# Optimization experiments

Measured on AMD Instinct MI355X. Metric: run time of the kernel, lower is better.

Reference implementation:

```python
import math
import jax, jax.numpy as jnp
import numpy as np

N = 1600; C_IN = 16; HID = 64; OUT = 64; D_K = 8; N_HEADS = 8
CUTS = 8; NUM_RBF = 8; RBF_PROJ = 4; RADIUS = 6.0; ALPHA = 3.0

def leaky(x):
    return jnp.where(x >= 0, x, 0.2 * x)

def group_norm(x, gamma, beta, groups=4, eps=1e-5):
    # x: [N, C]; torch GroupNorm applied on [1, C, N]: stats over (C/groups, N) per group
    n, c = x.shape
    xg = x.T.reshape(groups, -1)
    mu = jnp.mean(xg, axis=1, keepdims=True)
    var = jnp.mean((xg - mu) ** 2, axis=1, keepdims=True)
    xn = ((xg - mu) * jax.lax.rsqrt(var + eps)).reshape(c, n).T
    return xn * gamma + beta

def setup_inputs():
    key = jax.random.key(0)
    ks = jax.random.split(key, 32)
    def rn(k, shape, s=0.1):
        return (jax.random.normal(k, shape) * s).astype(jnp.float32)
    return {
        "points": jax.random.normal(ks[0], (N, 3), jnp.float32),
        "nuv": jax.random.normal(ks[1], (N, 3, 3), jnp.float32),
        "features": jax.random.normal(ks[2], (N, C_IN), jnp.float32),
        "w_in1": rn(ks[3], (HID, C_IN)), "b_in1": rn(ks[4], (HID,)),
        "w_in2": rn(ks[5], (HID, HID)), "b_in2": rn(ks[6], (HID,)),
        "g_in": 1.0 + rn(ks[7], (HID,)), "be_in": rn(ks[8], (HID,)),
        "wq": rn(ks[9], (HID, HID)), "bq": rn(ks[10], (HID,)),
        "wk": rn(ks[11], (HID, HID)), "bk": rn(ks[12], (HID,)),
        "wv": rn(ks[13], (HID, HID)), "bv": rn(ks[14], (HID,)),
        "conv_w1": rn(ks[15], (CUTS, 4 + RBF_PROJ), 0.5),
        "conv_b1": jnp.abs(rn(ks[16], (CUTS,), 0.5)),
        "conv_w2": rn(ks[17], (HID, CUTS), 0.3), "conv_b2": rn(ks[18], (HID,), 0.3),
        "rbf_log_sigma": jnp.log(jnp.asarray(0.6 * 2.0 / (NUM_RBF - 1), jnp.float32)),
        "rbf_a": rn(ks[19], (RBF_PROJ, NUM_RBF), 0.3), "rbf_b": rn(ks[20], (RBF_PROJ,), 0.1),
        "rbf_centers": jnp.linspace(0.0, 2.0, NUM_RBF, dtype=jnp.float32),
        "w_o1": rn(ks[21], (OUT, HID)), "b_o1": rn(ks[22], (OUT,)),
        "w_o2": rn(ks[23], (OUT, OUT)), "b_o2": rn(ks[24], (OUT,)),
        "g_out": 1.0 + rn(ks[25], (OUT,)), "be_out": rn(ks[26], (OUT,)),
        "w_res": rn(ks[27], (OUT, C_IN)), "b_res": rn(ks[28], (OUT,)),
    }

def reference(points, nuv, features, w_in1, b_in1, w_in2, b_in2, g_in, be_in,
              wq, bq, wk, bk, wv, bv, conv_w1, conv_b1, conv_w2, conv_b2,
              rbf_log_sigma, rbf_a, rbf_b, rbf_centers,
              w_o1, b_o1, w_o2, b_o2, g_out, be_out, w_res, b_res):
    # point-wise MLP + GroupNorm
    h = leaky(features @ w_in1.T + b_in1)
    h = leaky(h @ w_in2.T + b_in2)
    h = group_norm(h, g_in, be_in)
    Q = h @ wq.T + bq
    K = h @ wk.T + bk
    V = h @ wv.T + bv
    pts = points / (math.sqrt(2.0) * RADIUS)
    diff = pts[None, :, :] - pts[:, None, :]            # [N, N, 3] = x_j - x_i
    n_i = nuv[:, 0, :]
    n_j = jax.lax.stop_gradient(n_i)                    # j-side normals are detached in the original
    ndot = jnp.einsum("ia,ja->ij", n_i, n_j)            # <n_i, n_j>
    d2 = jnp.sum(diff ** 2, axis=-1) * (2.0 - ndot) ** 2  # pseudo-geodesic squared distance
    W = (1.0 + d2 / ALPHA) ** (-ALPHA)                  # geodesic window weight
    d2_safe = jnp.where(d2 > 0, d2, 1.0)
    base_d = jnp.where(d2 > 0, jnp.sqrt(d2_safe), 0.0)  # safe sqrt (finite grad at 0)
    sigma = jnp.maximum(jnp.exp(rbf_log_sigma), 1e-6)
    R = jnp.exp(-((base_d[:, :, None] - rbf_centers) ** 2) / (2.0 * sigma ** 2))  # [N,N,NUM_RBF]
    R_proj = R @ rbf_a.T + rbf_b                        # [N, N, RBF_PROJ]
    X_loc = jnp.einsum("iab,ijb->ija", nuv, diff)       # local tangent-frame coords [N,N,3]
    X = jnp.concatenate([X_loc, ndot[:, :, None], R_proj], axis=-1)  # [N, N, 4+RBF_PROJ]
    F1 = jax.nn.relu(X @ conv_w1.T + conv_b1)           # shared conv layer-1 [N, N, CUTS]
    scale = 1.0 / math.sqrt(D_K)
    heads = []
    for h_id in range(N_HEADS):
        s = slice(h_id * D_K, (h_id + 1) * D_K)
        Fh = jax.nn.relu(F1 @ conv_w2[s].T + conv_b2[s])      # per-head conv weights [N, N, D_K]
        S = (Q[:, s] @ K[:, s].T) * scale                     # attention logits [N, N]
        P = jax.nn.softmax(S, axis=1) * W                     # softmax over j, fused with window
        heads.append(jnp.einsum("ij,ijc,jc->ic", P, Fh, V[:, s]))
    agg = jnp.concatenate(heads, axis=1)                      # [N, HID]
    o = leaky(agg @ w_o1.T + b_o1)
    o = leaky(o @ w_o2.T + b_o2)
    o = group_norm(o, g_out, be_out)
    return o + features @ w_res.T + b_res
```

## Files before the change

kernel.cpp:

```cpp
#include <hip/hip_runtime.h>

#define NPTS 1600
#define NCHUNK 10
#define CHUNKJ 160
#define TILE 32
#define QS (0.35355339059327373f*1.4426950408889634f)
#define PSCALE 0.11785113019775793f

__device__ __forceinline__ float leaky(float x){ return x >= 0.f ? x : 0.2f*x; }
__device__ __forceinline__ float d4(float4 a, float4 b){ return a.x*b.x + a.y*b.y + a.z*b.z + a.w*b.w; }

__global__ __launch_bounds__(256) void k_in(
    const float* __restrict__ feat, const float* __restrict__ w1, const float* __restrict__ b1,
    const float* __restrict__ w2, const float* __restrict__ b2,
    const float* __restrict__ conv_w1, const float* __restrict__ conv_b1,
    const float* __restrict__ rbf_a, const float* __restrict__ rbf_b,
    float* __restrict__ h2out, float* __restrict__ stats,
    float* __restrict__ wrg, float* __restrict__ b1pg)
{
  __shared__ float sh[4][64];
  __shared__ float sred[4][8];
  int t = threadIdx.x, w = t>>6, c = t&63;
  int i = blockIdx.x*4 + w;

  if (blockIdx.x == 0) {
    if (t < 64) {
      int cc = t>>3, k = t&7; float s = 0.f;
      #pragma unroll
      for (int p=0;p<4;p++) s += conv_w1[cc*8+4+p]*rbf_a[p*8+k];
      wrg[t] = s;
    } else if (t < 72) {
      int cc = t-64; float s = conv_b1[cc];
      #pragma unroll
      for (int p=0;p<4;p++) s += conv_w1[cc*8+4+p]*rbf_b[p];
      b1pg[cc] = s;
    }
  }

  const float4* f4 = (const float4*)(feat + i*16);
  float4 f0=f4[0], f1v=f4[1], f2v=f4[2], f3v=f4[3];
  const float4* w1r = (const float4*)(w1 + c*16);
  float h1 = b1[c] + d4(f0,w1r[0]) + d4(f1v,w1r[1]) + d4(f2v,w1r[2]) + d4(f3v,w1r[3]);
  h1 = leaky(h1);
  sh[w][c] = h1;
  __syncthreads();
  float hh = b2[c];
  #pragma unroll
  for (int k4=0;k4<16;k4++){
    float4 hv = *(const float4*)&sh[w][k4*4];
    hh += d4(hv, *(const float4*)&w2[c*64 + k4*4]);
  }
  hh = leaky(hh);
  h2out[i*64+c] = hh;

  float s = hh, qq = hh*hh;
  s += __shfl_xor(s,1);  qq += __shfl_xor(qq,1);
  s += __shfl_xor(s,2);  qq += __shfl_xor(qq,2);
  s += __shfl_xor(s,4);  qq += __shfl_xor(qq,4);
  s += __shfl_xor(s,8);  qq += __shfl_xor(qq,8);
  if ((c&15)==0){ int g=c>>4; sred[w][g]=s; sred[w][4+g]=qq; }
  __syncthreads();
  if (t<8){ float v2 = sred[0][t]+sred[1][t]+sred[2][t]+sred[3][t]; atomicAdd(&stats[t], v2); }
}

__global__ __launch_bounds__(256) void k_qkv(
  const float* __restrict__ h2, const float* __restrict__ stats,
  const float* __restrict__ g_in, const float* __restrict__ be_in,
  const float* __restrict__ wq, const float* __restrict__ bq,
  const float* __restrict__ wk, const float* __restrict__ bk,
  const float* __restrict__ wv, const float* __restrict__ bv,
  float* __restrict__ Q, float* __restrict__ K, float* __restrict__ V)
{
  __shared__ float sh[4][64];
  int t=threadIdx.x, w=t>>6, c=t&63;
  int i = blockIdx.x*4 + w;
  int g = c>>4;
  const float inv = 1.f/25600.f;
  float mu = stats[g]*inv;
  float var = stats[4+g]*inv - mu*mu;
  float rs = rsqrtf(var + 1e-5f);
  float hn = (h2[i*64+c]-mu)*rs*g_in[c] + be_in[c];
  sh[w][c] = hn;
  __syncthreads();
  float q=bq[c], k=bk[c], v=bv[c];
  #pragma unroll
  for (int k4=0;k4<16;k4++){
    float4 hv = *(const float4*)&sh[w][k4*4];
    q += d4(hv, *(const float4*)&wq[c*64+k4*4]);
    k += d4(hv, *(const float4*)&wk[c*64+k4*4]);
    v += d4(hv, *(const float4*)&wv[c*64+k4*4]);
  }
  Q[i*64+c] = q*QS;
  K[i*64+c] = k;
  V[i*64+c] = v;
}

__global__ __launch_bounds__(256) void k_pair(
  const float* __restrict__ Qm, const float* __restrict__ Km, const float* __restrict__ Vm,
  const float* __restrict__ pts, const float* __restrict__ nuv,
  const float* __restrict__ w1, const float* __restrict__ wrg, const float* __restrict__ b1pg,
  const float* __restrict__ w2g, const float* __restrict__ b2g,
  const float* __restrict__ rbf_ls, const float* __restrict__ ceng,
  float* __restrict__ part)
{
  __shared__ __align__(16) float sQ[16][68];
  __shared__ __align__(16) float sWX[16][36];
  __shared__ __align__(16) float sKx[TILE][68];
  __shared__ __align__(16) float sVx[TILE][68];
  __shared__ __align__(16) float sPt[TILE][4];
  __shared__ __align__(16) float sNj[TILE][4];
  __shared__ __align__(16) float sRed[4][16][72];

  int t = threadIdx.x;
  int r = t & 15, jl = t >> 4;
  int bx = blockIdx.x;
  int rb = bx % 100, jc = bx / 100;
  int I0 = rb*16, J0 = jc*CHUNKJ;
  int i = I0 + r;

  {
    int row = t >> 4, col = (t & 15) << 2;
    *(float4*)&sQ[row][col] = *(const float4*)&Qm[(I0+row)*64 + col];
  }
  if (t < 128) {
    int r2 = t >> 3, cc = t & 7;
    int ib = (I0+r2)*9;
    #pragma unroll
    for (int b=0;b<3;b++)
      sWX[r2][cc*4+b] = w1[cc*8+0]*nuv[ib+b] + w1[cc*8+1]*nuv[ib+3+b] + w1[cc*8+2]*nuv[ib+6+b];
    sWX[r2][cc*4+3] = w1[cc*8+3];
  }

  float ls = rbf_ls[0];
  float sig = fmaxf(expf(ls), 1e-6f);
  float mexp = -1.4426950408889634f/(2.f*sig*sig);
  float cen[8];
  #pragma unroll
  for (int k=0;k<8;k++) cen[k] = ceng[k];

  float pix = pts[i*3+0]*PSCALE, piy = pts[i*3+1]*PSCALE, piz = pts[i*3+2]*PSCALE;
  float nix = nuv[i*9+0], niy = nuv[i*9+1], niz = nuv[i*9+2];

  float acc[64];
  #pragma unroll
  for (int o=0;o<64;o++) acc[o] = 0.f;
  float lh[8];
  #pragma unroll
  for (int h=0;h<8;h++) lh[h] = 0.f;

  #pragma unroll 1
  for (int tb=0; tb<CHUNKJ; tb+=TILE) {
    int jbase = J0 + tb;
    __syncthreads();
    #pragma unroll
    for (int qq2=0; qq2<2; qq2++) {
      int idx4 = t + qq2*256;
      int row = idx4 >> 4, col = (idx4 & 15) << 2;
      *(float4*)&sKx[row][col] = *(const float4*)&Km[(jbase+row)*64+col];
      *(float4*)&sVx[row][col] = *(const float4*)&Vm[(jbase+row)*64+col];
    }
    if (t < TILE) {
      int j = jbase + t;
      sPt[t][0]=pts[j*3+0]*PSCALE; sPt[t][1]=pts[j*3+1]*PSCALE; sPt[t][2]=pts[j*3+2]*PSCALE;
      sNj[t][0]=nuv[j*9+0]; sNj[t][1]=nuv[j*9+1]; sNj[t][2]=nuv[j*9+2];
    }
    __syncthreads();

    float F1[2][8], Wv[2];
    #pragma unroll
    for (int jj=0;jj<2;jj++) {
      int jloc = jl + (jj<<4);
      float dx = sPt[jloc][0]-pix, dy = sPt[jloc][1]-piy, dz = sPt[jloc][2]-piz;
      float ndot = nix*sNj[jloc][0] + niy*sNj[jloc][1] + niz*sNj[jloc][2];
      float d2r = dx*dx + dy*dy + dz*dz;
      float wf = 2.f - ndot;
      float d2 = d2r*wf*wf;
      float tp = fmaf(d2, 0.3333333333333333f, 1.f);
      Wv[jj] = __builtin_amdgcn_rcpf(tp*tp*tp);
      float dd = __builtin_amdgcn_sqrtf(d2);
      float R[8];
      #pragma unroll
      for (int k=0;k<8;k++){ float u = dd - cen[k]; R[k] = __builtin_amdgcn_exp2f(u*u*mexp); }
      #pragma unroll
      for (int cc=0;cc<8;cc++) {
        float4 wx = *(const float4*)&sWX[r][cc*4];
        float p = b1pg[cc] + wx.x*dx + wx.y*dy + wx.z*dz + wx.w*ndot;
        #pragma unroll
        for (int k=0;k<8;k++) p = fmaf(R[k], wrg[cc*8+k], p);
        F1[jj][cc] = fmaxf(p, 0.f);
      }
    }

    #pragma unroll
    for (int h=0;h<8;h++) {
      float4 q0 = *(const float4*)&sQ[r][h*8];
      float4 q1 = *(const float4*)&sQ[r][h*8+4];
      float ew[2];
      float va[2][8];
      #pragma unroll
      for (int jj=0;jj<2;jj++) {
        int jloc = jl + (jj<<4);
        float4 k0 = *(const float4*)&sKx[jloc][h*8];
        float4 k1 = *(const float4*)&sKx[jloc][h*8+4];
        float S = d4(q0,k0) + d4(q1,k1);
        float e = __builtin_amdgcn_exp2f(S);
        lh[h] += e;
        ew[jj] = e * Wv[jj];
        float4 v0 = *(const float4*)&sVx[jloc][h*8];
        float4 v1 = *(const float4*)&sVx[jloc][h*8+4];
        va[jj][0]=v0.x; va[jj][1]=v0.y; va[jj][2]=v0.z; va[jj][3]=v0.w;
        va[jj][4]=v1.x; va[jj][5]=v1.y; va[jj][6]=v1.z; va[jj][7]=v1.w;
      }
      #pragma unroll
      for (int cc=0;cc<8;cc++) {
        float b2v = b2g[h*8+cc];
        float w2v[8];
        #pragma unroll
        for (int b=0;b<8;b++) w2v[b] = w2g[(h*8+cc)*8+b];
        #pragma unroll
        for (int jj=0;jj<2;jj++) {
          float fh = b2v;
          #pragma unroll
          for (int b=0;b<8;b++) fh = fmaf(F1[jj][b], w2v[b], fh);
          fh = fmaxf(fh, 0.f);
          acc[h*8+cc] = fmaf(ew[jj]*fh, va[jj][cc], acc[h*8+cc]);
        }
      }
    }
  }

  #pragma unroll
  for (int o=0;o<64;o++){ acc[o] += __shfl_xor(acc[o],16); acc[o] += __shfl_xor(acc[o],32); }
  #pragma unroll
  for (int h=0;h<8;h++){ lh[h] += __shfl_xor(lh[h],16); lh[h] += __shfl_xor(lh[h],32); }
  __syncthreads();
  int wv = t >> 6, lane = t & 63;
  if (lane < 16) {
    #pragma unroll
    for (int o=0;o<64;o++) sRed[wv][lane][o] = acc[o];
    #pragma unroll
    for (int h=0;h<8;h++) sRed[wv][lane][64+h] = lh[h];
  }
  __syncthreads();
  for (int v2 = t; v2 < 16*72; v2 += 256) {
    int rr = v2/72, o = v2 - rr*72;
    float s = sRed[0][rr][o]+sRed[1][rr][o]+sRed[2][rr][o]+sRed[3][rr][o];
    part[(jc*NPTS + I0 + rr)*72 + o] = s;
  }
}

__global__ __launch_bounds__(256) void k_agg(
  const float* __restrict__ part, const float* __restrict__ w_o1, const float* __restrict__ b_o1,
  const float* __restrict__ w_o2, const float* __restrict__ b_o2,
  float* __restrict__ o2b, float* __restrict__ stats)
{
  __shared__ float sh[4][64];
  __shared__ float sred[4][8];
  int t = threadIdx.x, w = t>>6, c = t&63;
  int i = blockIdx.x*4 + w;
  int h = c>>3;
  float a = 0.f, L = 0.f;
  #pragma unroll 1
  for (int jc=0;jc<NCHUNK;jc++){
    const float* p = part + (jc*NPTS + i)*72;
    a += p[c]; L += p[64+h];
  }
  float agg = a / L;
  sh[w][c] = agg; __syncthreads();
  float o1 = b_o1[c];
  #pragma unroll
  for (int k4=0;k4<16;k4++){
    float4 hv = *(const float4*)&sh[w][k4*4];
    o1 += d4(hv, *(const float4*)&w_o1[c*64+k4*4]);
  }
  o1 = leaky(o1);
  __syncthreads();
  sh[w][c] = o1; __syncthreads();
  float o2 = b_o2[c];
  #pragma unroll
  for (int k4=0;k4<16;k4++){
    float4 hv = *(const float4*)&sh[w][k4*4];
    o2 += d4(hv, *(const float4*)&w_o2[c*64+k4*4]);
  }
  o2 = leaky(o2);
  o2b[i*64+c] = o2;

  float s = o2, qq = o2*o2;
  s += __shfl_xor(s,1);  qq += __shfl_xor(qq,1);
  s += __shfl_xor(s,2);  qq += __shfl_xor(qq,2);
  s += __shfl_xor(s,4);  qq += __shfl_xor(qq,4);
  s += __shfl_xor(s,8);  qq += __shfl_xor(qq,8);
  if ((c&15)==0){ int g=c>>4; sred[w][g]=s; sred[w][4+g]=qq; }
  __syncthreads();
  if (t<8){ float v2 = sred[0][t]+sred[1][t]+sred[2][t]+sred[3][t]; atomicAdd(&stats[8+t], v2); }
}

__global__ __launch_bounds__(256) void k_out(
  const float* __restrict__ o2b, const float* __restrict__ stats,
  const float* __restrict__ g_out, const float* __restrict__ be_out,
  const float* __restrict__ feat, const float* __restrict__ w_res, const float* __restrict__ b_res,
  float* __restrict__ out)
{
  int t = threadIdx.x, w = t>>6, c = t&63;
  int i = blockIdx.x*4 + w;
  int g = c>>4;
  const float inv = 1.f/25600.f;
  float mu = stats[8+g]*inv;
  float var = stats[12+g]*inv - mu*mu;
  float rs = rsqrtf(var + 1e-5f);
  float on = (o2b[i*64+c]-mu)*rs*g_out[c] + be_out[c];
  const float4* f4 = (const float4*)(feat + i*16);
  const float4* wr = (const float4*)(w_res + c*16);
  float res = b_res[c] + d4(f4[0],wr[0]) + d4(f4[1],wr[1]) + d4(f4[2],wr[2]) + d4(f4[3],wr[3]);
  out[i*64+c] = on + res;
}

extern "C" void kernel_launch(void* const* d_in, const int* in_sizes, int n_in,
                              void* d_out, int out_size, void* d_ws, size_t ws_size,
                              hipStream_t stream) {
  const float* points  = (const float*)d_in[0];
  const float* nuv     = (const float*)d_in[1];
  const float* feat    = (const float*)d_in[2];
  const float* w_in1   = (const float*)d_in[3];
  const float* b_in1   = (const float*)d_in[4];
  const float* w_in2   = (const float*)d_in[5];
  const float* b_in2   = (const float*)d_in[6];
  const float* g_in    = (const float*)d_in[7];
  const float* be_in   = (const float*)d_in[8];
  const float* wq      = (const float*)d_in[9];
  const float* bq      = (const float*)d_in[10];
  const float* wk      = (const float*)d_in[11];
  const float* bk      = (const float*)d_in[12];
  const float* wv      = (const float*)d_in[13];
  const float* bv      = (const float*)d_in[14];
  const float* conv_w1 = (const float*)d_in[15];
  const float* conv_b1 = (const float*)d_in[16];
  const float* conv_w2 = (const float*)d_in[17];
  const float* conv_b2 = (const float*)d_in[18];
  const float* rbf_ls  = (const float*)d_in[19];
  const float* rbf_a   = (const float*)d_in[20];
  const float* rbf_b   = (const float*)d_in[21];
  const float* rbf_c   = (const float*)d_in[22];
  const float* w_o1    = (const float*)d_in[23];
  const float* b_o1    = (const float*)d_in[24];
  const float* w_o2    = (const float*)d_in[25];
  const float* b_o2    = (const float*)d_in[26];
  const float* g_out   = (const float*)d_in[27];
  const float* be_out  = (const float*)d_in[28];
  const float* w_res   = (const float*)d_in[29];
  const float* b_res   = (const float*)d_in[30];

  float* ws    = (float*)d_ws;
  float* h2    = ws;
  float* Q     = ws + 102400;
  float* Km    = ws + 204800;
  float* V     = ws + 307200;
  float* stats = ws + 409600;
  float* wrg   = ws + 409616;
  float* b1pg  = ws + 409680;
  float* part  = ws + 409688;
  float* o2b   = ws + 1561688;
  float* out   = (float*)d_out;

  hipMemsetAsync(stats, 0, 16*sizeof(float), stream);
  k_in<<<400, 256, 0, stream>>>(feat, w_in1, b_in1, w_in2, b_in2,
                                conv_w1, conv_b1, rbf_a, rbf_b,
                                h2, stats, wrg, b1pg);
  k_qkv<<<400, 256, 0, stream>>>(h2, stats, g_in, be_in, wq, bq, wk, bk, wv, bv, Q, Km, V);
  k_pair<<<1000, 256, 0, stream>>>(Q, Km, V, points, nuv, conv_w1, wrg, b1pg,
                                   conv_w2, conv_b2, rbf_ls, rbf_c, part);
  k_agg<<<400, 256, 0, stream>>>(part, w_o1, b_o1, w_o2, b_o2, o2b, stats);
  k_out<<<400, 256, 0, stream>>>(o2b, stats, g_out, be_out, feat, w_res, b_res, out);
}
```

Measured before the change: 266.5 us.

## Use packed fp16 dot2 for pairwise conv layers and replace stat atomics

```diff
diff --git a/kernel.cpp b/kernel.cpp
--- a/kernel.cpp
+++ b/kernel.cpp
@@ -1,4 +1,7 @@
 #include <hip/hip_runtime.h>
+
+typedef __fp16 h2 __attribute__((ext_vector_type(2)));
+typedef unsigned int u32;
 
 #define NPTS 1600
 #define NCHUNK 10
@@ -6,17 +9,23 @@
 #define TILE 32
 #define QS (0.35355339059327373f*1.4426950408889634f)
 #define PSCALE 0.11785113019775793f
+#define LOG2E 1.4426950408889634f
 
 __device__ __forceinline__ float leaky(float x){ return x >= 0.f ? x : 0.2f*x; }
 __device__ __forceinline__ float d4(float4 a, float4 b){ return a.x*b.x + a.y*b.y + a.z*b.z + a.w*b.w; }
+__device__ __forceinline__ u32 pkn(float a, float b){ h2 v; v[0]=(__fp16)a; v[1]=(__fp16)b; return __builtin_bit_cast(u32,v); }
+__device__ __forceinline__ h2 u2h(u32 u){ return __builtin_bit_cast(h2,u); }
+__device__ __forceinline__ float dot2(h2 a, h2 b, float c){ return __builtin_amdgcn_fdot2(a,b,c,false); }
+__device__ __forceinline__ u32 rfl(u32 x){ return (u32)__builtin_amdgcn_readfirstlane((int)x); }
 
 __global__ __launch_bounds__(256) void k_in(
     const float* __restrict__ feat, const float* __restrict__ w1, const float* __restrict__ b1,
     const float* __restrict__ w2, const float* __restrict__ b2,
     const float* __restrict__ conv_w1, const float* __restrict__ conv_b1,
+    const float* __restrict__ conv_w2,
     const float* __restrict__ rbf_a, const float* __restrict__ rbf_b,
-    float* __restrict__ h2out, float* __restrict__ stats,
-    float* __restrict__ wrg, float* __restrict__ b1pg)
+    const float* __restrict__ rbf_ls, const float* __restrict__ rbf_c,
+    float* __restrict__ h2out, float* __restrict__ bstat1, float* __restrict__ wpk)
 {
   __shared__ float sh[4][64];
   __shared__ float sred[4][8];
@@ -24,16 +33,31 @@
   int i = blockIdx.x*4 + w;
 
   if (blockIdx.x == 0) {
-    if (t < 64) {
-      int cc = t>>3, k = t&7; float s = 0.f;
+    u32* wp = (u32*)wpk;
+    {
+      int row = t>>2, q = t&3;
+      wp[32 + row*4 + q] = pkn(conv_w2[row*8+2*q], conv_w2[row*8+2*q+1]);
+    }
+    if (t < 32) {
+      int cc = t>>2, kq = t&3;
+      float a0=0.f, a1=0.f;
       #pragma unroll
-      for (int p=0;p<4;p++) s += conv_w1[cc*8+4+p]*rbf_a[p*8+k];
-      wrg[t] = s;
-    } else if (t < 72) {
-      int cc = t-64; float s = conv_b1[cc];
+      for (int p=0;p<4;p++){ a0 += conv_w1[cc*8+4+p]*rbf_a[p*8+2*kq]; a1 += conv_w1[cc*8+4+p]*rbf_a[p*8+2*kq+1]; }
+      wp[cc*4+kq] = pkn(a0,a1);
+    } else if (t < 40) {
+      int cc = t-32; float s = conv_b1[cc];
       #pragma unroll
       for (int p=0;p<4;p++) s += conv_w1[cc*8+4+p]*rbf_b[p];
-      b1pg[cc] = s;
+      wpk[288+cc] = s;
+    } else if (t == 40) {
+      float sig = fmaxf(expf(rbf_ls[0]), 1e-6f);
+      float m = -LOG2E/(2.f*sig*sig);
+      float c0 = rbf_c[0];
+      float dl = rbf_c[1] - rbf_c[0];
+      wpk[296] = c0;
+      wpk[297] = m;
+      wpk[298] = -2.f*m*dl;
+      wpk[299] = m*dl*dl;
     }
   }
 
@@ -60,11 +84,11 @@
   s += __shfl_xor(s,8);  qq += __shfl_xor(qq,8);
   if ((c&15)==0){ int g=c>>4; sred[w][g]=s; sred[w][4+g]=qq; }
   __syncthreads();
-  if (t<8){ float v2 = sred[0][t]+sred[1][t]+sred[2][t]+sred[3][t]; atomicAdd(&stats[t], v2); }
+  if (t<8) bstat1[blockIdx.x*8+t] = sred[0][t]+sred[1][t]+sred[2][t]+sred[3][t];
 }
 
 __global__ __launch_bounds__(256) void k_qkv(
-  const float* __restrict__ h2, const float* __restrict__ stats,
+  const float* __restrict__ h2b, const float* __restrict__ bstat1,
   const float* __restrict__ g_in, const float* __restrict__ be_in,
   const float* __restrict__ wq, const float* __restrict__ bq,
   const float* __restrict__ wk, const float* __restrict__ bk,
@@ -72,14 +96,25 @@
   float* __restrict__ Q, float* __restrict__ K, float* __restrict__ V)
 {
   __shared__ float sh[4][64];
+  __shared__ float sp[64];
+  __shared__ float sst[8];
   int t=threadIdx.x, w=t>>6, c=t&63;
   int i = blockIdx.x*4 + w;
+  if (t<64){ int g=t&7; float s=0.f;
+    for (int m=t>>3; m<400; m+=8) s += bstat1[m*8+g];
+    sp[t]=s; }
+  __syncthreads();
+  if (t<8){ float s=0.f;
+    #pragma unroll
+    for (int q=0;q<8;q++) s += sp[q*8+t];
+    sst[t]=s; }
+  __syncthreads();
   int g = c>>4;
   const float inv = 1.f/25600.f;
-  float mu = stats[g]*inv;
-  float var = stats[4+g]*inv - mu*mu;
+  float mu = sst[g]*inv;
+  float var = sst[4+g]*inv - mu*mu;
   float rs = rsqrtf(var + 1e-5f);
-  float hn = (h2[i*64+c]-mu)*rs*g_in[c] + be_in[c];
+  float hn = (h2b[i*64+c]-mu)*rs*g_in[c] + be_in[c];
   sh[w][c] = hn;
   __syncthreads();
   float q=bq[c], k=bk[c], v=bv[c];
@@ -95,21 +130,20 @@
   V[i*64+c] = v;
 }
 
-__global__ __launch_bounds__(256) void k_pair(
+__global__ __launch_bounds__(256,4) void k_pair(
   const float* __restrict__ Qm, const float* __restrict__ Km, const float* __restrict__ Vm,
   const float* __restrict__ pts, const float* __restrict__ nuv,
-  const float* __restrict__ w1, const float* __restrict__ wrg, const float* __restrict__ b1pg,
-  const float* __restrict__ w2g, const float* __restrict__ b2g,
-  const float* __restrict__ rbf_ls, const float* __restrict__ ceng,
-  float* __restrict__ part)
+  const float* __restrict__ w1, const float* __restrict__ wpk,
+  const float* __restrict__ b2g, float* __restrict__ part)
 {
-  __shared__ __align__(16) float sQ[16][68];
-  __shared__ __align__(16) float sWX[16][36];
-  __shared__ __align__(16) float sKx[TILE][68];
-  __shared__ __align__(16) float sVx[TILE][68];
-  __shared__ __align__(16) float sPt[TILE][4];
-  __shared__ __align__(16) float sNj[TILE][4];
-  __shared__ __align__(16) float sRed[4][16][72];
+  __shared__ __align__(16) float SM[4928];
+  float* sQ  = SM;
+  float* sK  = SM + 1088;
+  u32*   sVp = (u32*)(SM + 3264);
+  u32*   sWX = (u32*)(SM + 4352);
+  float* sPt = SM + 4672;
+  float* sNj = SM + 4800;
+  float* sRed = SM;
 
   int t = threadIdx.x;
   int r = t & 15, jl = t >> 4;
@@ -118,25 +152,34 @@
   int I0 = rb*16, J0 = jc*CHUNKJ;
   int i = I0 + r;
 
-  {
-    int row = t >> 4, col = (t & 15) << 2;
-    *(float4*)&sQ[row][col] = *(const float4*)&Qm[(I0+row)*64 + col];
-  }
+  { int row = t>>4, col = (t&15)<<2;
+    *(float4*)&sQ[row*68+col] = *(const float4*)&Qm[(I0+row)*64 + col]; }
   if (t < 128) {
-    int r2 = t >> 3, cc = t & 7;
-    int ib = (I0+r2)*9;
-    #pragma unroll
-    for (int b=0;b<3;b++)
-      sWX[r2][cc*4+b] = w1[cc*8+0]*nuv[ib+b] + w1[cc*8+1]*nuv[ib+3+b] + w1[cc*8+2]*nuv[ib+6+b];
-    sWX[r2][cc*4+3] = w1[cc*8+3];
-  }
-
-  float ls = rbf_ls[0];
-  float sig = fmaxf(expf(ls), 1e-6f);
-  float mexp = -1.4426950408889634f/(2.f*sig*sig);
-  float cen[8];
-  #pragma unroll
-  for (int k=0;k<8;k++) cen[k] = ceng[k];
+    int r2 = t>>3, cc = t&7, ib = (I0+r2)*9;
+    float a0=w1[cc*8], a1=w1[cc*8+1], a2=w1[cc*8+2];
+    float x = a0*nuv[ib+0] + a1*nuv[ib+3] + a2*nuv[ib+6];
+    float y = a0*nuv[ib+1] + a1*nuv[ib+4] + a2*nuv[ib+7];
+    float z = a0*nuv[ib+2] + a1*nuv[ib+5] + a2*nuv[ib+8];
+    sWX[r2*20+cc*2+0] = pkn(x,y);
+    sWX[r2*20+cc*2+1] = pkn(z, w1[cc*8+3]);
+  }
+  __syncthreads();
+  u32 wxp[16];
+  #pragma unroll
+  for (int q2=0;q2<4;q2++) *(uint4*)&wxp[q2*4] = *(const uint4*)&sWX[r*20+q2*4];
+
+  const u32* wp = (const u32*)wpk;
+  h2 wr[8][4];
+  #pragma unroll
+  for (int cc=0;cc<8;cc++)
+    #pragma unroll
+    for (int q2=0;q2<4;q2++) wr[cc][q2] = u2h(rfl(wp[cc*4+q2]));
+  const u32* w2p = wp + 32;
+  const float* b1p = wpk + 288;
+  float c0  = wpk[296];
+  float mco = wpk[297];
+  float C2  = wpk[298];
+  float A1  = wpk[299];
 
   float pix = pts[i*3+0]*PSCALE, piy = pts[i*3+1]*PSCALE, piz = pts[i*3+2]*PSCALE;
   float nix = nuv[i*9+0], niy = nuv[i*9+1], niz = nuv[i*9+2];
@@ -153,78 +196,96 @@
     int jbase = J0 + tb;
     __syncthreads();
     #pragma unroll
-    for (int qq2=0; qq2<2; qq2++) {
-      int idx4 = t + qq2*256;
-      int row = idx4 >> 4, col = (idx4 & 15) << 2;
-      *(float4*)&sKx[row][col] = *(const float4*)&Km[(jbase+row)*64+col];
-      *(float4*)&sVx[row][col] = *(const float4*)&Vm[(jbase+row)*64+col];
+    for (int q2=0;q2<2;q2++) {
+      int idx = t + q2*256;
+      int row = idx >> 4, col = (idx & 15) << 2;
+      *(float4*)&sK[row*68+col] = *(const float4*)&Km[(jbase+row)*64+col];
+    }
+    { int row = t>>4, col = (t&15)<<2;
+      float4 a = *(const float4*)&Vm[(jbase+row)*64+col];
+      float4 b = *(const float4*)&Vm[(jbase+16+row)*64+col];
+      uint4 p; p.x=pkn(a.x,b.x); p.y=pkn(a.y,b.y); p.z=pkn(a.z,b.z); p.w=pkn(a.w,b.w);
+      *(uint4*)&sVp[row*68+col] = p;
     }
     if (t < TILE) {
       int j = jbase + t;
-      sPt[t][0]=pts[j*3+0]*PSCALE; sPt[t][1]=pts[j*3+1]*PSCALE; sPt[t][2]=pts[j*3+2]*PSCALE;
-      sNj[t][0]=nuv[j*9+0]; sNj[t][1]=nuv[j*9+1]; sNj[t][2]=nuv[j*9+2];
+      sPt[t*4+0]=pts[j*3+0]*PSCALE; sPt[t*4+1]=pts[j*3+1]*PSCALE; sPt[t*4+2]=pts[j*3+2]*PSCALE;
+      sNj[t*4+0]=nuv[j*9+0]; sNj[t*4+1]=nuv[j*9+1]; sNj[t*4+2]=nuv[j*9+2];
     }
     __syncthreads();
 
-    float F1[2][8], Wv[2];
+    h2 F1p[2][4];
+    float Wv[2];
     #pragma unroll
     for (int jj=0;jj<2;jj++) {
       int jloc = jl + (jj<<4);
-      float dx = sPt[jloc][0]-pix, dy = sPt[jloc][1]-piy, dz = sPt[jloc][2]-piz;
-      float ndot = nix*sNj[jloc][0] + niy*sNj[jloc][1] + niz*sNj[jloc][2];
+      float dx = sPt[jloc*4+0]-pix, dy = sPt[jloc*4+1]-piy, dz = sPt[jloc*4+2]-piz;
+      float ndot = nix*sNj[jloc*4+0] + niy*sNj[jloc*4+1] + niz*sNj[jloc*4+2];
       float d2r = dx*dx + dy*dy + dz*dz;
       float wf = 2.f - ndot;
       float d2 = d2r*wf*wf;
       float tp = fmaf(d2, 0.3333333333333333f, 1.f);
       Wv[jj] = __builtin_amdgcn_rcpf(tp*tp*tp);
       float dd = __builtin_amdgcn_sqrtf(d2);
+      float g0 = dd - c0;
+      float s2 = mco*g0*g0;
+      float uu = C2*g0;
       float R[8];
       #pragma unroll
-      for (int k=0;k<8;k++){ float u = dd - cen[k]; R[k] = __builtin_amdgcn_exp2f(u*u*mexp); }
+      for (int k=0;k<8;k++){
+        float kf = (float)k, k2f = (float)(k*k);
+        R[k] = __builtin_amdgcn_exp2f(fmaf(kf, uu, fmaf(k2f, A1, s2)));
+      }
+      h2 xv0; xv0[0]=(__fp16)dx; xv0[1]=(__fp16)dy;
+      h2 xv1; xv1[0]=(__fp16)dz; xv1[1]=(__fp16)ndot;
+      h2 r01=__builtin_amdgcn_cvt_pkrtz(R[0],R[1]);
+      h2 r23=__builtin_amdgcn_cvt_pkrtz(R[2],R[3]);
+      h2 r45=__builtin_amdgcn_cvt_pkrtz(R[4],R[5]);
+      h2 r67=__builtin_amdgcn_cvt_pkrtz(R[6],R[7]);
+      float F1f[8];
       #pragma unroll
-      for (int cc=0;cc<8;cc++) {
-        float4 wx = *(const float4*)&sWX[r][cc*4];
-        float p = b1pg[cc] + wx.x*dx + wx.y*dy + wx.z*dz + wx.w*ndot;
-        #pragma unroll
-        for (int k=0;k<8;k++) p = fmaf(R[k], wrg[cc*8+k], p);
-        F1[jj][cc] = fmaxf(p, 0.f);
+      for (int cc=0;cc<8;cc++){
+        float f = dot2(r67, wr[cc][3], b1p[cc]);
+        f = dot2(r45, wr[cc][2], f);
+        f = dot2(r23, wr[cc][1], f);
+        f = dot2(r01, wr[cc][0], f);
+        f = dot2(u2h(wxp[cc*2+1]), xv1, f);
+        f = dot2(u2h(wxp[cc*2+0]), xv0, f);
+        F1f[cc] = fmaxf(f, 0.f);
       }
+      F1p[jj][0]=__builtin_amdgcn_cvt_pkrtz(F1f[0],F1f[1]);
+      F1p[jj][1]=__builtin_amdgcn_cvt_pkrtz(F1f[2],F1f[3]);
+      F1p[jj][2]=__builtin_amdgcn_cvt_pkrtz(F1f[4],F1f[5]);
+      F1p[jj][3]=__builtin_amdgcn_cvt_pkrtz(F1f[6],F1f[7]);
     }
 
     #pragma unroll
     for (int h=0;h<8;h++) {
-      float4 q0 = *(const float4*)&sQ[r][h*8];
-      float4 q1 = *(const float4*)&sQ[r][h*8+4];
-      float ew[2];
-      float va[2][8];
+      float4 q0 = *(const float4*)&sQ[r*68+h*8];
+      float4 q1 = *(const float4*)&sQ[r*68+h*8+4];
+      float4 ka0 = *(const float4*)&sK[jl*68+h*8];
+      float4 ka1 = *(const float4*)&sK[jl*68+h*8+4];
+      float4 kb0 = *(const float4*)&sK[(jl+16)*68+h*8];
+      float4 kb1 = *(const float4*)&sK[(jl+16)*68+h*8+4];
+      float S0 = d4(q0,ka0) + d4(q1,ka1);
+      float S1 = d4(q0,kb0) + d4(q1,kb1);
+      float e0 = __builtin_amdgcn_exp2f(S0);
+      float e1 = __builtin_amdgcn_exp2f(S1);
+      lh[h] += e0 + e1;
+      h2 ewp; ewp[0]=(__fp16)(e0*Wv[0]); ewp[1]=(__fp16)(e1*Wv[1]);
+      uint4 vpA = *(const uint4*)&sVp[jl*68+h*8];
+      uint4 vpB = *(const uint4*)&sVp[jl*68+h*8+4];
+      u32 vparr[8] = {vpA.x,vpA.y,vpA.z,vpA.w,vpB.x,vpB.y,vpB.z,vpB.w};
       #pragma unroll
-      for (int jj=0;jj<2;jj++) {
-        int jloc = jl + (jj<<4);
-        float4 k0 = *(const float4*)&sKx[jloc][h*8];
-        float4 k1 = *(const float4*)&sKx[jloc][h*8+4];
-        float S = d4(q0,k0) + d4(q1,k1);
-        float e = __builtin_amdgcn_exp2f(S);
-        lh[h] += e;
-        ew[jj] = e * Wv[jj];
-        float4 v0 = *(const float4*)&sVx[jloc][h*8];
-        float4 v1 = *(const float4*)&sVx[jloc][h*8+4];
-        va[jj][0]=v0.x; va[jj][1]=v0.y; va[jj][2]=v0.z; va[jj][3]=v0.w;
-        va[jj][4]=v1.x; va[jj][5]=v1.y; va[jj][6]=v1.z; va[jj][7]=v1.w;
-      }
-      #pragma unroll
-      for (int cc=0;cc<8;cc++) {
-        float b2v = b2g[h*8+cc];
-        float w2v[8];
-        #pragma unroll
-        for (int b=0;b<8;b++) w2v[b] = w2g[(h*8+cc)*8+b];
-        #pragma unroll
-        for (int jj=0;jj<2;jj++) {
-          float fh = b2v;
-          #pragma unroll
-          for (int b=0;b<8;b++) fh = fmaf(F1[jj][b], w2v[b], fh);
-          fh = fmaxf(fh, 0.f);
-          acc[h*8+cc] = fmaf(ew[jj]*fh, va[jj][cc], acc[h*8+cc]);
-        }
+      for (int cc=0;cc<8;cc++){
+        int rw = h*8+cc;
+        h2 w0=u2h(w2p[rw*4+0]), w1h=u2h(w2p[rw*4+1]), w2h=u2h(w2p[rw*4+2]), w3h=u2h(w2p[rw*4+3]);
+        float b2v = b2g[rw];
+        float fh0 = dot2(F1p[0][0],w0, dot2(F1p[0][1],w1h, dot2(F1p[0][2],w2h, dot2(F1p[0][3],w3h, b2v))));
+        float fh1 = dot2(F1p[1][0],w0, dot2(F1p[1][1],w1h, dot2(F1p[1][2],w2h, dot2(F1p[1][3],w3h, b2v))));
+        h2 fhp = __builtin_amdgcn_cvt_pkrtz(fmaxf(fh0,0.f), fmaxf(fh1,0.f));
+        h2 ev = u2h(vparr[cc]) * ewp;
+        acc[rw] = dot2(fhp, ev, acc[rw]);
       }
     }
   }
@@ -237,22 +298,22 @@
   int wv = t >> 6, lane = t & 63;
   if (lane < 16) {
     #pragma unroll
-    for (int o=0;o<64;o++) sRed[wv][lane][o] = acc[o];
-    #pragma unroll
-    for (int h=0;h<8;h++) sRed[wv][lane][64+h] = lh[h];
+    for (int o=0;o<64;o++) sRed[(wv*16+lane)*72+o] = acc[o];
+    #pragma unroll
+    for (int h=0;h<8;h++) sRed[(wv*16+lane)*72+64+h] = lh[h];
   }
   __syncthreads();
   for (int v2 = t; v2 < 16*72; v2 += 256) {
     int rr = v2/72, o = v2 - rr*72;
-    float s = sRed[0][rr][o]+sRed[1][rr][o]+sRed[2][rr][o]+sRed[3][rr][o];
-    part[(jc*NPTS + I0 + rr)*72 + o] = s;
+    part[(jc*NPTS + I0 + rr)*72 + o] =
+      sRed[(0*16+rr)*72+o] + sRed[(1*16+rr)*72+o] + sRed[(2*16+rr)*72+o] + sRed[(3*16+rr)*72+o];
   }
 }
 
 __global__ __launch_bounds__(256) void k_agg(
   const float* __restrict__ part, const float* __restrict__ w_o1, const float* __restrict__ b_o1,
   const float* __restrict__ w_o2, const float* __restrict__ b_o2,
-  float* __restrict__ o2b, float* __restrict__ stats)
+  float* __restrict__ o2b, float* __restrict__ bstat2)
 {
   __shared__ float sh[4][64];
   __shared__ float sred[4][8];
@@ -260,7 +321,7 @@
   int i = blockIdx.x*4 + w;
   int h = c>>3;
   float a = 0.f, L = 0.f;
-  #pragma unroll 1
+  #pragma unroll
   for (int jc=0;jc<NCHUNK;jc++){
     const float* p = part + (jc*NPTS + i)*72;
     a += p[c]; L += p[64+h];
@@ -292,21 +353,32 @@
   s += __shfl_xor(s,8);  qq += __shfl_xor(qq,8);
   if ((c&15)==0){ int g=c>>4; sred[w][g]=s; sred[w][4+g]=qq; }
   __syncthreads();
-  if (t<8){ float v2 = sred[0][t]+sred[1][t]+sred[2][t]+sred[3][t]; atomicAdd(&stats[8+t], v2); }
+  if (t<8) bstat2[blockIdx.x*8+t] = sred[0][t]+sred[1][t]+sred[2][t]+sred[3][t];
 }
 
 __global__ __launch_bounds__(256) void k_out(
-  const float* __restrict__ o2b, const float* __restrict__ stats,
+  const float* __restrict__ o2b, const float* __restrict__ bstat2,
   const float* __restrict__ g_out, const float* __restrict__ be_out,
   const float* __restrict__ feat, const float* __restrict__ w_res, const float* __restrict__ b_res,
   float* __restrict__ out)
 {
+  __shared__ float sp[64];
+  __shared__ float sst[8];
   int t = threadIdx.x, w = t>>6, c = t&63;
   int i = blockIdx.x*4 + w;
+  if (t<64){ int g=t&7; float s=0.f;
+    for (int m=t>>3; m<400; m+=8) s += bstat2[m*8+g];
+    sp[t]=s; }
+  __syncthreads();
+  if (t<8){ float s=0.f;
+    #pragma unroll
+    for (int q=0;q<8;q++) s += sp[q*8+t];
+    sst[t]=s; }
+  __syncthreads();
   int g = c>>4;
   const float inv = 1.f/25600.f;
-  float mu = stats[8+g]*inv;
-  float var = stats[12+g]*inv - mu*mu;
+  float mu = sst[g]*inv;
+  float var = sst[4+g]*inv - mu*mu;
   float rs = rsqrtf(var + 1e-5f);
   float on = (o2b[i*64+c]-mu)*rs*g_out[c] + be_out[c];
   const float4* f4 = (const float4*)(feat + i*16);
@@ -350,25 +422,23 @@
   const float* w_res   = (const float*)d_in[29];
   const float* b_res   = (const float*)d_in[30];
 
-  float* ws    = (float*)d_ws;
-  float* h2    = ws;
-  float* Q     = ws + 102400;
-  float* Km    = ws + 204800;
-  float* V     = ws + 307200;
-  float* stats = ws + 409600;
-  float* wrg   = ws + 409616;
-  float* b1pg  = ws + 409680;
-  float* part  = ws + 409688;
-  float* o2b   = ws + 1561688;
-  float* out   = (float*)d_out;
-
-  hipMemsetAsync(stats, 0, 16*sizeof(float), stream);
+  float* ws     = (float*)d_ws;
+  float* h2f    = ws;
+  float* Qb     = ws + 102400;
+  float* Kb     = ws + 204800;
+  float* Vb     = ws + 307200;
+  float* bstat1 = ws + 409600;
+  float* bstat2 = ws + 412800;
+  float* wpk    = ws + 416000;
+  float* part   = ws + 416320;
+  float* o2b    = ws + 1568320;
+  float* out    = (float*)d_out;
+
   k_in<<<400, 256, 0, stream>>>(feat, w_in1, b_in1, w_in2, b_in2,
-                                conv_w1, conv_b1, rbf_a, rbf_b,
-                                h2, stats, wrg, b1pg);
-  k_qkv<<<400, 256, 0, stream>>>(h2, stats, g_in, be_in, wq, bq, wk, bk, wv, bv, Q, Km, V);
-  k_pair<<<1000, 256, 0, stream>>>(Q, Km, V, points, nuv, conv_w1, wrg, b1pg,
-                                   conv_w2, conv_b2, rbf_ls, rbf_c, part);
-  k_agg<<<400, 256, 0, stream>>>(part, w_o1, b_o1, w_o2, b_o2, o2b, stats);
-  k_out<<<400, 256, 0, stream>>>(o2b, stats, g_out, be_out, feat, w_res, b_res, out);
-}
+                                conv_w1, conv_b1, conv_w2, rbf_a, rbf_b, rbf_ls, rbf_c,
+                                h2f, bstat1, wpk);
+  k_qkv<<<400, 256, 0, stream>>>(h2f, bstat1, g_in, be_in, wq, bq, wk, bk, wv, bv, Qb, Kb, Vb);
+  k_pair<<<1000, 256, 0, stream>>>(Qb, Kb, Vb, points, nuv, conv_w1, wpk, conv_b2, part);
+  k_agg<<<400, 256, 0, stream>>>(part, w_o1, b_o1, w_o2, b_o2, o2b, bstat2);
+  k_out<<<400, 256, 0, stream>>>(o2b, bstat2, g_out, be_out, feat, w_res, b_res, out);
+}
```

Measured after the change: 270.1 us. About the same (+1.3%).
